# Kernel optimization log

Hardware: AMD Instinct MI355X
Metric: run time of the kernel (lower is better)

The kernel has to match this reference:

```python
import jax, jax.numpy as jnp
import numpy as np

B, S, D_IN = 16, 512, 768
HID, OUT = 64, 12
NEG = 1e12


def setup_inputs() -> dict:
    key = jax.random.key(0)
    k1, k2, k3 = jax.random.split(key, 3)
    x = jax.random.normal(k1, (B, S, D_IN), dtype=jnp.float32)
    mask = jnp.ones((B, S), dtype=jnp.float32)
    W = jax.random.normal(k2, (D_IN, HID * OUT * 2), dtype=jnp.float32) * 0.02
    b = jax.random.normal(k3, (HID * OUT * 2,), dtype=jnp.float32) * 0.02
    return {"x": x, "mask": mask, "W": W, "b": b}


def reference(x, mask, W, b):
    Bb, Ss, _ = x.shape
    h, out = HID, OUT
    # QKV-style projection, split into `out` heads of 2h each
    proj = (x @ W + b).reshape(Bb, Ss, out, 2 * h)  # [b, s, out, 2h]
    qw, kw = proj[..., :h], proj[..., h:]           # [b, s, out, h]

    # Sinusoidal position embedding (merge='zero'): interleaved sin/cos
    pos_ids = jnp.arange(Ss, dtype=x.dtype)
    inv_freq = jnp.power(10000.0, -2.0 * jnp.arange(h // 2, dtype=x.dtype) / h)
    ang = pos_ids[:, None] * inv_freq               # [s, h/2]
    sin, cos = jnp.sin(ang), jnp.cos(ang)
    # torch: pos[..., None, 1::2].repeat(1,1,1,2) -> TILED (not interleaved)
    cos_pos = jnp.concatenate([cos, cos], axis=-1)[None, :, None, :]  # [1, s, 1, h]
    sin_pos = jnp.concatenate([sin, sin], axis=-1)[None, :, None, :]

    def rope(w):
        # stack([-w_odd, w_even], -1).reshape -> interleaved rotation partner
        w2 = jnp.stack([-w[..., 1::2], w[..., ::2]], axis=-1).reshape(w.shape)
        return w * cos_pos + w2 * sin_pos

    qw = rope(qw)
    kw = rope(kw)

    logits = jnp.einsum('bmhd,bnhd->bhmn', qw, kw)  # [b, out, s, s]

    pad = mask[:, None, None, :]                    # broadcast over [b, out, s, s]
    logits = logits * pad - (1.0 - pad) * NEG

    tril = jnp.tril(jnp.ones((Ss, Ss), dtype=logits.dtype), -1)
    logits = logits - tril * NEG

    return logits / (h ** 0.5)
```

## Files before the change

kernel.cpp:

```cpp
#include <hip/hip_runtime.h>
#include <stdint.h>

#define DIN   768
#define NPROJ 1536
#define SEQ   512
#define NHEAD 12
#define NBATCH 16
#define NEGV  1000000000000.0f

typedef short bf16x8 __attribute__((ext_vector_type(8)));
typedef float f32x4  __attribute__((ext_vector_type(4)));

__device__ __forceinline__ unsigned short f2bf(float f) {
    union { float f; unsigned int u; } v; v.f = f;
    return (unsigned short)((v.u + 0x7FFFu + ((v.u >> 16) & 1u)) >> 16);
}
__device__ __forceinline__ float bf2f(unsigned int u) {
    union { unsigned int u; float f; } v; v.u = u << 16;
    return v.f;
}

__global__ void k_wt(const float* __restrict__ W, unsigned short* __restrict__ Wt) {
    __shared__ float tile[32][33];
    int n0 = blockIdx.x * 32, k0 = blockIdx.y * 32;
    int tx = threadIdx.x, ty = threadIdx.y;
    tile[ty][tx] = W[(size_t)(k0 + ty) * NPROJ + n0 + tx];
    __syncthreads();
    Wt[(size_t)(n0 + ty) * DIN + k0 + tx] = f2bf(tile[tx][ty]);
}

__global__ __launch_bounds__(256) void k_gemm(const float* __restrict__ X,
                                              const unsigned short* __restrict__ Wt,
                                              const float* __restrict__ bias,
                                              unsigned short* __restrict__ P) {
    __shared__ unsigned short sA[128][72];
    __shared__ unsigned short sB[128][72];
    const int tid = threadIdx.x;
    const int m0 = blockIdx.y * 128, n0 = blockIdx.x * 128;
    const int lane = tid & 63, w = tid >> 6;
    const int q = lane >> 4, r = lane & 15;
    const int wm = w >> 1, wn = w & 1;
    f32x4 acc[4][4];
#pragma unroll
    for (int i = 0; i < 4; i++)
#pragma unroll
        for (int j = 0; j < 4; j++) acc[i][j] = (f32x4){0.f, 0.f, 0.f, 0.f};

    for (int k0 = 0; k0 < DIN; k0 += 64) {
        __syncthreads();
#pragma unroll
        for (int it = 0; it < 8; it++) {
            int c = tid + it * 256;
            int row = c >> 4, col = (c & 15) * 4;
            float4 v = *(const float4*)&X[(size_t)(m0 + row) * DIN + k0 + col];
            short4 sv;
            sv.x = (short)f2bf(v.x); sv.y = (short)f2bf(v.y);
            sv.z = (short)f2bf(v.z); sv.w = (short)f2bf(v.w);
            *(short4*)&sA[row][col] = sv;
        }
#pragma unroll
        for (int it = 0; it < 4; it++) {
            int c = tid + it * 256;
            int row = c >> 3, col = (c & 7) * 8;
            *(int4*)&sB[row][col] = *(const int4*)&Wt[(size_t)(n0 + row) * DIN + k0 + col];
        }
        __syncthreads();
#pragma unroll
        for (int kk = 0; kk < 64; kk += 32) {
            bf16x8 af[4], bfr[4];
#pragma unroll
            for (int t = 0; t < 4; t++)
                af[t] = *(const bf16x8*)&sA[wm * 64 + t * 16 + r][kk + q * 8];
#pragma unroll
            for (int t = 0; t < 4; t++)
                bfr[t] = *(const bf16x8*)&sB[wn * 64 + t * 16 + r][kk + q * 8];
#pragma unroll
            for (int tm = 0; tm < 4; tm++)
#pragma unroll
                for (int tn = 0; tn < 4; tn++)
                    acc[tm][tn] = __builtin_amdgcn_mfma_f32_16x16x32_bf16(
                        af[tm], bfr[tn], acc[tm][tn], 0, 0, 0);
        }
    }
#pragma unroll
    for (int tn = 0; tn < 4; tn++) {
        int gn = n0 + wn * 64 + tn * 16 + r;
        float bb = bias[gn];
#pragma unroll
        for (int tm = 0; tm < 4; tm++) {
            int gm = m0 + wm * 64 + tm * 16 + q * 4;
#pragma unroll
            for (int i = 0; i < 4; i++)
                P[(size_t)(gm + i) * NPROJ + gn] = f2bf(acc[tm][tn][i] + bb);
        }
    }
}

__global__ void k_rope(unsigned short* __restrict__ P) {
    const int t = blockIdx.x * 256 + threadIdx.x;
    const int row = t >> 4;
    const int fe = (t & 15) * 2;
    const float s = (float)(row & (SEQ - 1));
    const float C = 0.41524101186092034f;
    float sn0, cs0, sn1, cs1;
    sincosf(s * exp2f(-(float)fe * C), &sn0, &cs0);
    sincosf(s * exp2f(-(float)(fe + 1) * C), &sn1, &cs1);
    unsigned short* rowp = P + (size_t)row * NPROJ;
#pragma unroll
    for (int v = 0; v < 24; v++) {
#pragma unroll
        for (int dd = 0; dd < 2; dd++) {
            unsigned int* ap = (unsigned int*)(rowp + v * 64 + fe + dd * 32);
            unsigned int pk = *ap;
            float w0 = bf2f(pk & 0xFFFFu);
            float w1 = bf2f(pk >> 16);
            float o0 = w0 * cs0 - w1 * sn0;
            float o1 = w1 * cs1 + w0 * sn1;
            *ap = (unsigned int)f2bf(o0) | ((unsigned int)f2bf(o1) << 16);
        }
    }
}

__global__ __launch_bounds__(256) void k_attn(const unsigned short* __restrict__ P,
                                              const float* __restrict__ mask,
                                              float* __restrict__ out) {
    __shared__ unsigned short sQ[128][72];
    __shared__ unsigned short sK[128][72];
    const int tid = threadIdx.x;
    const int b = blockIdx.z, h = blockIdx.y;
    const int mt = blockIdx.x >> 2, nt = blockIdx.x & 3;
#pragma unroll
    for (int it = 0; it < 4; it++) {
        int c = tid + it * 256;
        int row = c >> 3, col = (c & 7) * 8;
        size_t gq = (size_t)(b * SEQ + mt * 128 + row) * NPROJ + h * 128 + col;
        *(int4*)&sQ[row][col] = *(const int4*)&P[gq];
        size_t gk = (size_t)(b * SEQ + nt * 128 + row) * NPROJ + h * 128 + 64 + col;
        *(int4*)&sK[row][col] = *(const int4*)&P[gk];
    }
    __syncthreads();
    const int lane = tid & 63, w = tid >> 6;
    const int q = lane >> 4, r = lane & 15;
    const int wm = w >> 1, wn = w & 1;
    f32x4 acc[4][4];
#pragma unroll
    for (int i = 0; i < 4; i++)
#pragma unroll
        for (int j = 0; j < 4; j++) acc[i][j] = (f32x4){0.f, 0.f, 0.f, 0.f};
#pragma unroll
    for (int kk = 0; kk < 64; kk += 32) {
        bf16x8 af[4], bfr[4];
#pragma unroll
        for (int t = 0; t < 4; t++)
            af[t] = *(const bf16x8*)&sQ[wm * 64 + t * 16 + r][kk + q * 8];
#pragma unroll
        for (int t = 0; t < 4; t++)
            bfr[t] = *(const bf16x8*)&sK[wn * 64 + t * 16 + r][kk + q * 8];
#pragma unroll
        for (int tm = 0; tm < 4; tm++)
#pragma unroll
            for (int tn = 0; tn < 4; tn++)
                acc[tm][tn] = __builtin_amdgcn_mfma_f32_16x16x32_bf16(
                    af[tm], bfr[tn], acc[tm][tn], 0, 0, 0);
    }
    float padv[4];
    int gns[4];
#pragma unroll
    for (int tn = 0; tn < 4; tn++) {
        gns[tn] = nt * 128 + wn * 64 + tn * 16 + r;
        padv[tn] = mask[b * SEQ + gns[tn]];
    }
#pragma unroll
    for (int tm = 0; tm < 4; tm++) {
        int gm = mt * 128 + wm * 64 + tm * 16 + q * 4;
#pragma unroll
        for (int i = 0; i < 4; i++) {
            int m = gm + i;
            float* orow = out + ((size_t)((b * NHEAD + h) * SEQ + m)) * SEQ;
#pragma unroll
            for (int tn = 0; tn < 4; tn++) {
                float v = acc[tm][tn][i];
                float pv = padv[tn];
                v = v * pv - (1.f - pv) * NEGV;
                if (gns[tn] < m) v -= NEGV;
                orow[gns[tn]] = v * 0.125f;
            }
        }
    }
}

extern "C" void kernel_launch(void* const* d_in, const int* in_sizes, int n_in,
                              void* d_out, int out_size, void* d_ws, size_t ws_size,
                              hipStream_t stream) {
    const float* x    = (const float*)d_in[0];
    const float* mask = (const float*)d_in[1];
    const float* W    = (const float*)d_in[2];
    const float* bias = (const float*)d_in[3];
    float* out = (float*)d_out;

    unsigned short* Wt = (unsigned short*)d_ws;
    unsigned short* P  = Wt + (size_t)NPROJ * DIN;

    k_wt  <<<dim3(NPROJ / 32, DIN / 32), dim3(32, 32), 0, stream>>>(W, Wt);
    k_gemm<<<dim3(NPROJ / 128, (NBATCH * SEQ) / 128), 256, 0, stream>>>(x, Wt, bias, P);
    k_rope<<<(NBATCH * SEQ * 16) / 256, 256, 0, stream>>>(P);
    k_attn<<<dim3(16, NHEAD, NBATCH), 256, 0, stream>>>(P, mask, out);
}
```

Baseline: 284.2 us.

## Vectorize stores via LDS staging, precast X to bf16, restructure RoPE and transpose

The attention epilogue and the GEMM epilogue now stage accumulators in shared memory and write rows with 16-byte vector stores instead of scattered scalar stores. The mask is also read as float4. X gets its own bf16 cast kernel when the workspace is large enough, so GEMM tiles load bf16 directly. RoPE computes sin/cos once per position into shared memory and processes 8 elements per thread with vector loads. The weight transpose uses 64x64 tiles with float4 reads and int4 writes. These changes target uncoalesced writes of the large fp32 output and redundant conversion work, at the cost of extra barriers and an extra kernel launch.

```diff
diff --git a/kernel.cpp b/kernel.cpp
--- a/kernel.cpp
+++ b/kernel.cpp
@@ -15,26 +15,54 @@
     union { float f; unsigned int u; } v; v.f = f;
     return (unsigned short)((v.u + 0x7FFFu + ((v.u >> 16) & 1u)) >> 16);
 }
-__device__ __forceinline__ float bf2f(unsigned int u) {
-    union { unsigned int u; float f; } v; v.u = u << 16;
+__device__ __forceinline__ float bf2f(unsigned short u) {
+    union { unsigned int u; float f; } v; v.u = ((unsigned int)u) << 16;
     return v.f;
 }
 
-__global__ void k_wt(const float* __restrict__ W, unsigned short* __restrict__ Wt) {
-    __shared__ float tile[32][33];
-    int n0 = blockIdx.x * 32, k0 = blockIdx.y * 32;
-    int tx = threadIdx.x, ty = threadIdx.y;
-    tile[ty][tx] = W[(size_t)(k0 + ty) * NPROJ + n0 + tx];
-    __syncthreads();
-    Wt[(size_t)(n0 + ty) * DIN + k0 + tx] = f2bf(tile[tx][ty]);
-}
-
+__global__ __launch_bounds__(256) void k_xcast(const float* __restrict__ X,
+                                               unsigned short* __restrict__ Xb) {
+    int i = (blockIdx.x * 256 + threadIdx.x) * 4;
+    float4 v = *(const float4*)&X[i];
+    short4 s;
+    s.x = (short)f2bf(v.x); s.y = (short)f2bf(v.y);
+    s.z = (short)f2bf(v.z); s.w = (short)f2bf(v.w);
+    *(short4*)&Xb[i] = s;
+}
+
+__global__ __launch_bounds__(256) void k_wt(const float* __restrict__ W,
+                                            unsigned short* __restrict__ Wt) {
+    __shared__ unsigned short T[64][72];
+    const int n0 = blockIdx.x * 64, k0 = blockIdx.y * 64;
+    const int tid = threadIdx.x;
+#pragma unroll
+    for (int it = 0; it < 4; it++) {
+        int c = tid + it * 256;
+        int kl = c >> 4, nl = (c & 15) * 4;
+        float4 v = *(const float4*)&W[(size_t)(k0 + kl) * NPROJ + n0 + nl];
+        T[nl + 0][kl] = f2bf(v.x);
+        T[nl + 1][kl] = f2bf(v.y);
+        T[nl + 2][kl] = f2bf(v.z);
+        T[nl + 3][kl] = f2bf(v.w);
+    }
+    __syncthreads();
+#pragma unroll
+    for (int it = 0; it < 2; it++) {
+        int c = tid + it * 256;
+        int nl = c >> 3, kb = (c & 7) * 8;
+        *(int4*)&Wt[(size_t)(n0 + nl) * DIN + k0 + kb] = *(int4*)&T[nl][kb];
+    }
+}
+
+template <bool PRE>
 __global__ __launch_bounds__(256) void k_gemm(const float* __restrict__ X,
+                                              const unsigned short* __restrict__ Xb,
                                               const unsigned short* __restrict__ Wt,
                                               const float* __restrict__ bias,
                                               unsigned short* __restrict__ P) {
-    __shared__ unsigned short sA[128][72];
-    __shared__ unsigned short sB[128][72];
+    __shared__ unsigned short smem[2 * 128 * 72];
+    unsigned short* sA = smem;
+    unsigned short* sB = smem + 128 * 72;
     const int tid = threadIdx.x;
     const int m0 = blockIdx.y * 128, n0 = blockIdx.x * 128;
     const int lane = tid & 63, w = tid >> 6;
@@ -48,21 +76,32 @@
 
     for (int k0 = 0; k0 < DIN; k0 += 64) {
         __syncthreads();
-#pragma unroll
-        for (int it = 0; it < 8; it++) {
-            int c = tid + it * 256;
-            int row = c >> 4, col = (c & 15) * 4;
-            float4 v = *(const float4*)&X[(size_t)(m0 + row) * DIN + k0 + col];
-            short4 sv;
-            sv.x = (short)f2bf(v.x); sv.y = (short)f2bf(v.y);
-            sv.z = (short)f2bf(v.z); sv.w = (short)f2bf(v.w);
-            *(short4*)&sA[row][col] = sv;
+        if (PRE) {
+#pragma unroll
+            for (int it = 0; it < 4; it++) {
+                int c = tid + it * 256;
+                int row = c >> 3, col = (c & 7) * 8;
+                *(int4*)&sA[row * 72 + col] =
+                    *(const int4*)&Xb[(size_t)(m0 + row) * DIN + k0 + col];
+            }
+        } else {
+#pragma unroll
+            for (int it = 0; it < 8; it++) {
+                int c = tid + it * 256;
+                int row = c >> 4, col = (c & 15) * 4;
+                float4 v = *(const float4*)&X[(size_t)(m0 + row) * DIN + k0 + col];
+                short4 sv;
+                sv.x = (short)f2bf(v.x); sv.y = (short)f2bf(v.y);
+                sv.z = (short)f2bf(v.z); sv.w = (short)f2bf(v.w);
+                *(short4*)&sA[row * 72 + col] = sv;
+            }
         }
 #pragma unroll
         for (int it = 0; it < 4; it++) {
             int c = tid + it * 256;
             int row = c >> 3, col = (c & 7) * 8;
-            *(int4*)&sB[row][col] = *(const int4*)&Wt[(size_t)(n0 + row) * DIN + k0 + col];
+            *(int4*)&sB[row * 72 + col] =
+                *(const int4*)&Wt[(size_t)(n0 + row) * DIN + k0 + col];
         }
         __syncthreads();
 #pragma unroll
@@ -70,10 +109,10 @@
             bf16x8 af[4], bfr[4];
 #pragma unroll
             for (int t = 0; t < 4; t++)
-                af[t] = *(const bf16x8*)&sA[wm * 64 + t * 16 + r][kk + q * 8];
+                af[t] = *(const bf16x8*)&sA[(wm * 64 + t * 16 + r) * 72 + kk + q * 8];
 #pragma unroll
             for (int t = 0; t < 4; t++)
-                bfr[t] = *(const bf16x8*)&sB[wn * 64 + t * 16 + r][kk + q * 8];
+                bfr[t] = *(const bf16x8*)&sB[(wn * 64 + t * 16 + r) * 72 + kk + q * 8];
 #pragma unroll
             for (int tm = 0; tm < 4; tm++)
 #pragma unroll
@@ -82,50 +121,72 @@
                         af[tm], bfr[tn], acc[tm][tn], 0, 0, 0);
         }
     }
-#pragma unroll
-    for (int tn = 0; tn < 4; tn++) {
-        int gn = n0 + wn * 64 + tn * 16 + r;
-        float bb = bias[gn];
-#pragma unroll
-        for (int tm = 0; tm < 4; tm++) {
-            int gm = m0 + wm * 64 + tm * 16 + q * 4;
+    float bb[4];
+#pragma unroll
+    for (int tn = 0; tn < 4; tn++) bb[tn] = bias[n0 + wn * 64 + tn * 16 + r];
+    __syncthreads();
+    unsigned short* sT = smem;
+#pragma unroll
+    for (int tm = 0; tm < 4; tm++) {
+        int rowb = wm * 64 + tm * 16 + q * 4;
+#pragma unroll
+        for (int tn = 0; tn < 4; tn++) {
+            int col = wn * 64 + tn * 16 + r;
 #pragma unroll
             for (int i = 0; i < 4; i++)
-                P[(size_t)(gm + i) * NPROJ + gn] = f2bf(acc[tm][tn][i] + bb);
-        }
-    }
-}
-
-__global__ void k_rope(unsigned short* __restrict__ P) {
-    const int t = blockIdx.x * 256 + threadIdx.x;
-    const int row = t >> 4;
-    const int fe = (t & 15) * 2;
-    const float s = (float)(row & (SEQ - 1));
-    const float C = 0.41524101186092034f;
-    float sn0, cs0, sn1, cs1;
-    sincosf(s * exp2f(-(float)fe * C), &sn0, &cs0);
-    sincosf(s * exp2f(-(float)(fe + 1) * C), &sn1, &cs1);
-    unsigned short* rowp = P + (size_t)row * NPROJ;
-#pragma unroll
-    for (int v = 0; v < 24; v++) {
-#pragma unroll
-        for (int dd = 0; dd < 2; dd++) {
-            unsigned int* ap = (unsigned int*)(rowp + v * 64 + fe + dd * 32);
-            unsigned int pk = *ap;
-            float w0 = bf2f(pk & 0xFFFFu);
-            float w1 = bf2f(pk >> 16);
-            float o0 = w0 * cs0 - w1 * sn0;
-            float o1 = w1 * cs1 + w0 * sn1;
-            *ap = (unsigned int)f2bf(o0) | ((unsigned int)f2bf(o1) << 16);
-        }
+                sT[(rowb + i) * 136 + col] = f2bf(acc[tm][tn][i] + bb[tn]);
+        }
+    }
+    __syncthreads();
+#pragma unroll
+    for (int it = 0; it < 8; it++) {
+        int c = tid + it * 256;
+        int row = c >> 4, colb = (c & 15) * 8;
+        *(int4*)&P[(size_t)(m0 + row) * NPROJ + n0 + colb] =
+            *(int4*)&sT[row * 136 + colb];
+    }
+}
+
+__global__ __launch_bounds__(256) void k_rope(unsigned short* __restrict__ P) {
+    const int s = blockIdx.x;
+    const int tid = threadIdx.x;
+    __shared__ float cs[32], sn[32];
+    if (tid < 32) {
+        const float C = 0.41524101186092034f;
+        float a = (float)s * exp2f(-(float)tid * C);
+        sincosf(a, &sn[tid], &cs[tid]);
+    }
+    __syncthreads();
+#pragma unroll
+    for (int it = 0; it < 12; it++) {
+        int idx = tid + it * 256;
+        int bb = idx / 192, c = idx % 192;
+        unsigned short* p = P + (size_t)(bb * SEQ + s) * NPROJ + c * 8;
+        union { int4 v; unsigned short u[8]; } pk;
+        pk.v = *(const int4*)p;
+        int d0 = (c & 7) * 8;
+        float wv[8];
+#pragma unroll
+        for (int j = 0; j < 8; j++) wv[j] = bf2f(pk.u[j]);
+#pragma unroll
+        for (int pr = 0; pr < 4; pr++) {
+            int je = (d0 + 2 * pr) & 31;
+            int jo = je + 1;
+            float oe = wv[2 * pr] * cs[je] - wv[2 * pr + 1] * sn[je];
+            float oo = wv[2 * pr + 1] * cs[jo] + wv[2 * pr] * sn[jo];
+            pk.u[2 * pr]     = f2bf(oe);
+            pk.u[2 * pr + 1] = f2bf(oo);
+        }
+        *(int4*)p = pk.v;
     }
 }
 
 __global__ __launch_bounds__(256) void k_attn(const unsigned short* __restrict__ P,
                                               const float* __restrict__ mask,
                                               float* __restrict__ out) {
-    __shared__ unsigned short sQ[128][72];
-    __shared__ unsigned short sK[128][72];
+    __shared__ unsigned short smem[2 * 128 * 72];
+    unsigned short* sQ = smem;
+    unsigned short* sK = smem + 128 * 72;
     const int tid = threadIdx.x;
     const int b = blockIdx.z, h = blockIdx.y;
     const int mt = blockIdx.x >> 2, nt = blockIdx.x & 3;
@@ -134,9 +195,9 @@
         int c = tid + it * 256;
         int row = c >> 3, col = (c & 7) * 8;
         size_t gq = (size_t)(b * SEQ + mt * 128 + row) * NPROJ + h * 128 + col;
-        *(int4*)&sQ[row][col] = *(const int4*)&P[gq];
+        *(int4*)&sQ[row * 72 + col] = *(const int4*)&P[gq];
         size_t gk = (size_t)(b * SEQ + nt * 128 + row) * NPROJ + h * 128 + 64 + col;
-        *(int4*)&sK[row][col] = *(const int4*)&P[gk];
+        *(int4*)&sK[row * 72 + col] = *(const int4*)&P[gk];
     }
     __syncthreads();
     const int lane = tid & 63, w = tid >> 6;
@@ -152,10 +213,10 @@
         bf16x8 af[4], bfr[4];
 #pragma unroll
         for (int t = 0; t < 4; t++)
-            af[t] = *(const bf16x8*)&sQ[wm * 64 + t * 16 + r][kk + q * 8];
+            af[t] = *(const bf16x8*)&sQ[(wm * 64 + t * 16 + r) * 72 + kk + q * 8];
 #pragma unroll
         for (int t = 0; t < 4; t++)
-            bfr[t] = *(const bf16x8*)&sK[wn * 64 + t * 16 + r][kk + q * 8];
+            bfr[t] = *(const bf16x8*)&sK[(wn * 64 + t * 16 + r) * 72 + kk + q * 8];
 #pragma unroll
         for (int tm = 0; tm < 4; tm++)
 #pragma unroll
@@ -163,28 +224,33 @@
                 acc[tm][tn] = __builtin_amdgcn_mfma_f32_16x16x32_bf16(
                     af[tm], bfr[tn], acc[tm][tn], 0, 0, 0);
     }
-    float padv[4];
-    int gns[4];
-#pragma unroll
-    for (int tn = 0; tn < 4; tn++) {
-        gns[tn] = nt * 128 + wn * 64 + tn * 16 + r;
-        padv[tn] = mask[b * SEQ + gns[tn]];
-    }
+    float* sbuf = (float*)smem;
+    const int rowb = wm * 16 + q * 4;
 #pragma unroll
     for (int tm = 0; tm < 4; tm++) {
-        int gm = mt * 128 + wm * 64 + tm * 16 + q * 4;
-#pragma unroll
-        for (int i = 0; i < 4; i++) {
-            int m = gm + i;
-            float* orow = out + ((size_t)((b * NHEAD + h) * SEQ + m)) * SEQ;
-#pragma unroll
-            for (int tn = 0; tn < 4; tn++) {
-                float v = acc[tm][tn][i];
-                float pv = padv[tn];
-                v = v * pv - (1.f - pv) * NEGV;
-                if (gns[tn] < m) v -= NEGV;
-                orow[gns[tn]] = v * 0.125f;
-            }
+        __syncthreads();
+#pragma unroll
+        for (int tn = 0; tn < 4; tn++) {
+            int col = wn * 64 + tn * 16 + r;
+#pragma unroll
+            for (int i = 0; i < 4; i++)
+                sbuf[(rowb + i) * 132 + col] = acc[tm][tn][i];
+        }
+        __syncthreads();
+#pragma unroll
+        for (int it = 0; it < 4; it++) {
+            int c = tid + it * 256;
+            int rl = c >> 5, cb = (c & 31) * 4;
+            float4 v = *(float4*)&sbuf[rl * 132 + cb];
+            int m = mt * 128 + (rl >> 4) * 64 + tm * 16 + (rl & 15);
+            int n = nt * 128 + cb;
+            float4 mk = *(const float4*)&mask[b * SEQ + n];
+            float4 o;
+            o.x = (v.x * mk.x - (1.f - mk.x) * NEGV - ((n + 0) < m ? NEGV : 0.f)) * 0.125f;
+            o.y = (v.y * mk.y - (1.f - mk.y) * NEGV - ((n + 1) < m ? NEGV : 0.f)) * 0.125f;
+            o.z = (v.z * mk.z - (1.f - mk.z) * NEGV - ((n + 2) < m ? NEGV : 0.f)) * 0.125f;
+            o.w = (v.w * mk.w - (1.f - mk.w) * NEGV - ((n + 3) < m ? NEGV : 0.f)) * 0.125f;
+            *(float4*)&out[((size_t)((b * NHEAD + h) * SEQ + m)) * SEQ + n] = o;
         }
     }
 }
@@ -198,11 +264,23 @@
     const float* bias = (const float*)d_in[3];
     float* out = (float*)d_out;
 
+    const size_t wtN = (size_t)NPROJ * DIN;
+    const size_t pN  = (size_t)NBATCH * SEQ * NPROJ;
+    const size_t xN  = (size_t)NBATCH * SEQ * DIN;
     unsigned short* Wt = (unsigned short*)d_ws;
-    unsigned short* P  = Wt + (size_t)NPROJ * DIN;
-
-    k_wt  <<<dim3(NPROJ / 32, DIN / 32), dim3(32, 32), 0, stream>>>(W, Wt);
-    k_gemm<<<dim3(NPROJ / 128, (NBATCH * SEQ) / 128), 256, 0, stream>>>(x, Wt, bias, P);
-    k_rope<<<(NBATCH * SEQ * 16) / 256, 256, 0, stream>>>(P);
+    unsigned short* P  = Wt + wtN;
+    unsigned short* Xb = P + pN;
+    const bool pre = ws_size >= (wtN + pN + xN) * sizeof(unsigned short);
+
+    k_wt<<<dim3(NPROJ / 64, DIN / 64), 256, 0, stream>>>(W, Wt);
+    if (pre) {
+        k_xcast<<<(int)(xN / (256 * 4)), 256, 0, stream>>>(x, Xb);
+        k_gemm<true><<<dim3(NPROJ / 128, (NBATCH * SEQ) / 128), 256, 0, stream>>>(
+            x, Xb, Wt, bias, P);
+    } else {
+        k_gemm<false><<<dim3(NPROJ / 128, (NBATCH * SEQ) / 128), 256, 0, stream>>>(
+            x, nullptr, Wt, bias, P);
+    }
+    k_rope<<<SEQ, 256, 0, stream>>>(P);
     k_attn<<<dim3(16, NHEAD, NBATCH), 256, 0, stream>>>(P, mask, out);
 }
```

New measurement: 280.1 us. Within noise of the previous version (-1.4%).
